# Kernel tuning notes

Hardware: AMD Instinct MI355X
Metric: run time of the kernel (lower is better)

Reference implementation:

```python
import jax, jax.numpy as jnp
import numpy as np

B, T, D, S = 32, 4096, 512, 256
SCALE = 0.1  # time_bias_scale


def setup_inputs() -> dict:
    key = jax.random.key(0)
    ks = jax.random.split(key, 9)
    return {
        "context": jax.random.normal(ks[0], (B, T, D), jnp.float32),
        "t_star": jax.random.uniform(ks[1], (B,), jnp.float32),
        "t_context": jax.random.uniform(ks[2], (B, T, 1), jnp.float32),
        "W1": jax.random.normal(ks[3], (1, D), jnp.float32) / np.sqrt(1.0),
        "b1": jax.random.normal(ks[4], (D,), jnp.float32) * 0.02,
        "W2": jax.random.normal(ks[5], (D, D), jnp.float32) / np.sqrt(D),
        "b2": jax.random.normal(ks[6], (D,), jnp.float32) * 0.02,
        "Wout": jax.random.normal(ks[7], (D, 2 * S), jnp.float32) / np.sqrt(D),
        "bout": jax.random.normal(ks[8], (2 * S,), jnp.float32) * 0.02,
    }


def reference(context, t_star, t_context, W1, b1, W2, b2, Wout, bout):
    # query embed: Linear(1,D) -> SiLU -> Linear(D,D)
    h = jax.nn.silu(t_star[:, None] @ W1 + b1)        # (B, D)
    q = h @ W2 + b2                                   # (B, D)
    # single-query attention scores with additive time bias
    scores = jnp.einsum('bd,btd->bt', q, context)     # (B, T)
    time_bias = -jnp.abs(t_star[:, None] - t_context[..., 0]) / SCALE  # (B, T)
    weights = jax.nn.softmax(scores + time_bias, axis=-1)
    pooled = jnp.einsum('bt,btd->bd', weights, context)  # (B, D)
    out = pooled @ Wout + bout                            # (B, 2S)
    mu, log_sigma = out[:, :S], out[:, S:]
    return (mu, log_sigma)
```

## Files before the change

### kernel.cpp

```cpp
#include <hip/hip_runtime.h>
#include <math.h>

#define BB 32
#define TT 4096
#define DD 512
#define SS 256
#define SEG 128
#define GRP 16
static constexpr float INV_SCALE = 10.0f;

__global__ __launch_bounds__(512) void k_q(
    const float* __restrict__ t_star, const float* __restrict__ W1,
    const float* __restrict__ b1, const float* __restrict__ W2,
    const float* __restrict__ b2, float* __restrict__ q) {
  const int b   = blockIdx.x >> 3;
  const int jg  = blockIdx.x & 7;
  const int tid = threadIdx.x;
  const int di  = tid & 63;
  const int kg  = tid >> 6;
  __shared__ float h[DD];
  __shared__ float red[8][64];
  {
    float x = t_star[b] * W1[tid] + b1[tid];
    h[tid] = x / (1.0f + __expf(-x));
  }
  __syncthreads();
  const float* w = W2 + jg * 64 + di;
  float acc = 0.0f;
#pragma unroll 8
  for (int kk = 0; kk < 64; ++kk) {
    const int k = kg * 64 + kk;
    acc += h[k] * w[(size_t)k * DD];
  }
  red[kg][di] = acc;
  __syncthreads();
  if (tid < 64) {
    float s = 0.0f;
#pragma unroll
    for (int g = 0; g < 8; ++g) s += red[g][tid];
    q[b * DD + jg * 64 + tid] = s + b2[jg * 64 + tid];
  }
}

#define GLDS(gp, lp)                                                        \
  __builtin_amdgcn_global_load_lds(                                         \
      (const __attribute__((address_space(1))) void*)(gp),                  \
      (__attribute__((address_space(3))) void*)(lp), 16, 0, 0)

__global__ __launch_bounds__(256) void k_fused(
    const float* __restrict__ ctx, const float* __restrict__ q,
    const float* __restrict__ t_star, const float* __restrict__ t_ctx,
    float* __restrict__ part_pool,
    float* __restrict__ part_ms) {
  __shared__ __align__(16) float lds[4][3][2 * DD];
  const int wid  = threadIdx.x >> 6;
  const int lane = threadIdx.x & 63;
  const int w    = blockIdx.x * 4 + wid;
  const int b    = w >> 7;
  const int s    = w & 127;

  const float4* qp = (const float4*)(q + b * DD);
  const float4 q0 = qp[lane];
  const float4 q1 = qp[64 + lane];
  const float ts = t_star[b];
  const float2 tc = *(const float2*)(t_ctx + b * TT + ((lane & 15) * 2 * SEG + 2 * s));
  const float tbx = -fabsf(ts - tc.x) * INV_SCALE;
  const float tby = -fabsf(ts - tc.y) * INV_SCALE;

  float m = -INFINITY, l = 0.0f;
  float4 p0 = {0, 0, 0, 0}, p1 = {0, 0, 0, 0};

  const float* cb = ctx + ((size_t)b * TT + 2 * s) * DD;

#pragma unroll
  for (int g = 0; g < 2; ++g) {
    const float* gb = cb + (size_t)g * 2 * SEG * DD;
    float* sb = &lds[wid][g][0];
#pragma unroll
    for (int piece = 0; piece < 4; ++piece)
      GLDS(gb + piece * 256 + lane * 4, sb + piece * 256);
  }

#pragma unroll
  for (int g = 0; g < GRP; ++g) {
    if (g + 2 < GRP) {
      const float* gb = cb + (size_t)(g + 2) * 2 * SEG * DD;
      float* sb = &lds[wid][(g + 2) % 3][0];
#pragma unroll
      for (int piece = 0; piece < 4; ++piece)
        GLDS(gb + piece * 256 + lane * 4, sb + piece * 256);
      asm volatile("s_waitcnt vmcnt(8)" ::: "memory");
    } else if (g + 1 < GRP) {
      asm volatile("s_waitcnt vmcnt(4)" ::: "memory");
    } else {
      asm volatile("s_waitcnt vmcnt(0)" ::: "memory");
    }

    const float4* sf = (const float4*)&lds[wid][g % 3][0];
    const float4 x0 = sf[lane];
    const float4 x1 = sf[64 + lane];
    const float4 y0 = sf[128 + lane];
    const float4 y1 = sf[192 + lane];

    float s0 = x0.x * q0.x + x0.y * q0.y + x0.z * q0.z + x0.w * q0.w +
               x1.x * q1.x + x1.y * q1.y + x1.z * q1.z + x1.w * q1.w;
    float s1 = y0.x * q0.x + y0.y * q0.y + y0.z * q0.z + y0.w * q0.w +
               y1.x * q1.x + y1.y * q1.y + y1.z * q1.z + y1.w * q1.w;
#pragma unroll
    for (int off = 32; off > 0; off >>= 1) {
      s0 += __shfl_xor(s0, off);
      s1 += __shfl_xor(s1, off);
    }
    s0 += __shfl(tbx, g);
    s1 += __shfl(tby, g);

    const float gm = fmaxf(s0, s1);
    const float nm = fmaxf(m, gm);
    const float sc = __expf(m - nm);
    m = nm;
    const float e0 = __expf(s0 - m);
    const float e1 = __expf(s1 - m);
    l = l * sc + e0 + e1;
    p0.x = p0.x * sc + e0 * x0.x + e1 * y0.x;
    p0.y = p0.y * sc + e0 * x0.y + e1 * y0.y;
    p0.z = p0.z * sc + e0 * x0.z + e1 * y0.z;
    p0.w = p0.w * sc + e0 * x0.w + e1 * y0.w;
    p1.x = p1.x * sc + e0 * x1.x + e1 * y1.x;
    p1.y = p1.y * sc + e0 * x1.y + e1 * y1.y;
    p1.z = p1.z * sc + e0 * x1.z + e1 * y1.z;
    p1.w = p1.w * sc + e0 * x1.w + e1 * y1.w;
  }

  float4* pp = (float4*)(part_pool + (size_t)w * DD);
  pp[lane] = p0;
  pp[64 + lane] = p1;
  if (lane == 0) {
    part_ms[w * 2 + 0] = m;
    part_ms[w * 2 + 1] = l;
  }
}

__global__ __launch_bounds__(512) void k_merge(
    const float* __restrict__ part_pool, const float* __restrict__ part_ms,
    float* __restrict__ pool) {
  const int b   = blockIdx.x >> 2;
  const int dg  = blockIdx.x & 3;
  const int tid = threadIdx.x;
  const int lane = tid & 63;
  const int base = b * SEG;
  __shared__ float scl[SEG];
  __shared__ float red[4][128];

  const float mA = part_ms[(base + lane) * 2 + 0];
  const float mB = part_ms[(base + 64 + lane) * 2 + 0];
  const float lA = part_ms[(base + lane) * 2 + 1];
  const float lB = part_ms[(base + 64 + lane) * 2 + 1];
  float M = fmaxf(mA, mB);
#pragma unroll
  for (int off = 32; off > 0; off >>= 1) M = fmaxf(M, __shfl_xor(M, off));
  float Z = __expf(mA - M) * lA + __expf(mB - M) * lB;
#pragma unroll
  for (int off = 32; off > 0; off >>= 1) Z += __shfl_xor(Z, off);
  const float invZ = 1.0f / Z;
  if (tid < SEG) scl[tid] = __expf(part_ms[(base + tid) * 2] - M);
  __syncthreads();

  const int dl = tid & 127;
  const int cg = tid >> 7;
  float acc = 0.0f;
#pragma unroll 8
  for (int i = 0; i < 32; ++i) {
    const int c = cg * 32 + i;
    acc += scl[c] * part_pool[((size_t)base + c) * DD + dg * 128 + dl];
  }
  red[cg][dl] = acc;
  __syncthreads();
  if (tid < 128)
    pool[b * DD + dg * 128 + tid] =
        (red[0][tid] + red[1][tid] + red[2][tid] + red[3][tid]) * invZ;
}

__global__ __launch_bounds__(256) void k_out(
    const float* __restrict__ pool, const float* __restrict__ Wout,
    const float* __restrict__ bout, float* __restrict__ out) {
  const int b   = blockIdx.x >> 3;
  const int jg  = blockIdx.x & 7;
  const int tid = threadIdx.x;
  const int kg  = tid >> 6;
  const int j   = tid & 63;
  const int jc  = jg * 64 + j;
  __shared__ float p[DD];
  __shared__ float red[4][64];

  p[tid] = pool[b * DD + tid];
  p[tid + 256] = pool[b * DD + 256 + tid];
  __syncthreads();

  float acc = 0.0f;
#pragma unroll 8
  for (int kk = 0; kk < 128; ++kk) {
    const int k = kg * 128 + kk;
    acc += p[k] * Wout[(size_t)k * DD + jc];
  }
  red[kg][j] = acc;
  __syncthreads();
  if (tid < 64) {
    const int jj = jg * 64 + tid;
    float o = red[0][tid] + red[1][tid] + red[2][tid] + red[3][tid] + bout[jj];
    if (jj < SS) out[b * SS + jj] = o;
    else         out[BB * SS + b * SS + (jj - SS)] = o;
  }
}

extern "C" void kernel_launch(void* const* d_in, const int* in_sizes, int n_in,
                              void* d_out, int out_size, void* d_ws, size_t ws_size,
                              hipStream_t stream) {
  const float* ctx    = (const float*)d_in[0];
  const float* t_star = (const float*)d_in[1];
  const float* t_ctx  = (const float*)d_in[2];
  const float* W1     = (const float*)d_in[3];
  const float* b1     = (const float*)d_in[4];
  const float* W2     = (const float*)d_in[5];
  const float* b2     = (const float*)d_in[6];
  const float* Wout   = (const float*)d_in[7];
  const float* bout   = (const float*)d_in[8];
  float* out = (float*)d_out;

  float* ws = (float*)d_ws;
  float* q         = ws;
  float* part_pool = q + (size_t)BB * DD;
  float* part_ms   = part_pool + (size_t)BB * SEG * DD;
  float* pool      = part_ms + (size_t)BB * SEG * 2;

  k_q<<<BB * 8, 512, 0, stream>>>(t_star, W1, b1, W2, b2, q);
  k_fused<<<BB * SEG / 4, 256, 0, stream>>>(ctx, q, t_star, t_ctx, part_pool, part_ms);
  k_merge<<<BB * 4, 512, 0, stream>>>(part_pool, part_ms, pool);
  k_out<<<BB * 8, 256, 0, stream>>>(pool, Wout, bout, out);
}
```

Baseline: 73.12 us.

## Process one context row per step with deeper 5-slot async prefetch pipeline

Each wave now handles one row per iteration instead of a pair, over 32 iterations, with a 5-slot LDS ring and 4 rows in flight instead of 3 slots holding pairs. Rows are strided by SEG instead of pairs strided by 2*SEG, and the time-bias lookup and vmcnt wait ladder change to match. The aim is smaller, more numerous in-flight loads and a simpler per-step softmax update. In exchange there are twice as many shuffle reductions and online-softmax rescales per row, and fewer bytes are in flight per wave.

Measured after the change: 76.51 us. 1.05x slower.

```diff
diff --git a/kernel.cpp b/kernel.cpp
--- a/kernel.cpp
+++ b/kernel.cpp
@@ -6,7 +6,7 @@
 #define DD 512
 #define SS 256
 #define SEG 128
-#define GRP 16
+#define GRP 32
 static constexpr float INV_SCALE = 10.0f;
 
 __global__ __launch_bounds__(512) void k_q(
@@ -52,7 +52,7 @@
     const float* __restrict__ t_star, const float* __restrict__ t_ctx,
     float* __restrict__ part_pool,
     float* __restrict__ part_ms) {
-  __shared__ __align__(16) float lds[4][3][2 * DD];
+  __shared__ __align__(16) float lds[4][5][DD];
   const int wid  = threadIdx.x >> 6;
   const int lane = threadIdx.x & 63;
   const int w    = blockIdx.x * 4 + wid;
@@ -63,72 +63,63 @@
   const float4 q0 = qp[lane];
   const float4 q1 = qp[64 + lane];
   const float ts = t_star[b];
-  const float2 tc = *(const float2*)(t_ctx + b * TT + ((lane & 15) * 2 * SEG + 2 * s));
-  const float tbx = -fabsf(ts - tc.x) * INV_SCALE;
-  const float tby = -fabsf(ts - tc.y) * INV_SCALE;
+  const float tcv = t_ctx[b * TT + (lane & 31) * SEG + s];
+  const float tb = -fabsf(ts - tcv) * INV_SCALE;
 
   float m = -INFINITY, l = 0.0f;
   float4 p0 = {0, 0, 0, 0}, p1 = {0, 0, 0, 0};
 
-  const float* cb = ctx + ((size_t)b * TT + 2 * s) * DD;
-
-#pragma unroll
-  for (int g = 0; g < 2; ++g) {
-    const float* gb = cb + (size_t)g * 2 * SEG * DD;
+  const float* cb = ctx + ((size_t)b * TT + s) * DD;
+
+#pragma unroll
+  for (int g = 0; g < 4; ++g) {
+    const float* gb = cb + (size_t)g * SEG * DD;
     float* sb = &lds[wid][g][0];
-#pragma unroll
-    for (int piece = 0; piece < 4; ++piece)
-      GLDS(gb + piece * 256 + lane * 4, sb + piece * 256);
+    GLDS(gb + lane * 4, sb);
+    GLDS(gb + 256 + lane * 4, sb + 256);
   }
 
 #pragma unroll
   for (int g = 0; g < GRP; ++g) {
-    if (g + 2 < GRP) {
-      const float* gb = cb + (size_t)(g + 2) * 2 * SEG * DD;
-      float* sb = &lds[wid][(g + 2) % 3][0];
-#pragma unroll
-      for (int piece = 0; piece < 4; ++piece)
-        GLDS(gb + piece * 256 + lane * 4, sb + piece * 256);
+    if (g + 4 < GRP) {
+      const float* gb = cb + (size_t)(g + 4) * SEG * DD;
+      float* sb = &lds[wid][(g + 4) % 5][0];
+      GLDS(gb + lane * 4, sb);
+      GLDS(gb + 256 + lane * 4, sb + 256);
       asm volatile("s_waitcnt vmcnt(8)" ::: "memory");
-    } else if (g + 1 < GRP) {
+    } else if (g + 4 == GRP) {
+      asm volatile("s_waitcnt vmcnt(6)" ::: "memory");
+    } else if (g + 4 == GRP + 1) {
       asm volatile("s_waitcnt vmcnt(4)" ::: "memory");
+    } else if (g + 4 == GRP + 2) {
+      asm volatile("s_waitcnt vmcnt(2)" ::: "memory");
     } else {
       asm volatile("s_waitcnt vmcnt(0)" ::: "memory");
     }
 
-    const float4* sf = (const float4*)&lds[wid][g % 3][0];
+    const float4* sf = (const float4*)&lds[wid][g % 5][0];
     const float4 x0 = sf[lane];
     const float4 x1 = sf[64 + lane];
-    const float4 y0 = sf[128 + lane];
-    const float4 y1 = sf[192 + lane];
-
-    float s0 = x0.x * q0.x + x0.y * q0.y + x0.z * q0.z + x0.w * q0.w +
-               x1.x * q1.x + x1.y * q1.y + x1.z * q1.z + x1.w * q1.w;
-    float s1 = y0.x * q0.x + y0.y * q0.y + y0.z * q0.z + y0.w * q0.w +
-               y1.x * q1.x + y1.y * q1.y + y1.z * q1.z + y1.w * q1.w;
-#pragma unroll
-    for (int off = 32; off > 0; off >>= 1) {
-      s0 += __shfl_xor(s0, off);
-      s1 += __shfl_xor(s1, off);
-    }
-    s0 += __shfl(tbx, g);
-    s1 += __shfl(tby, g);
-
-    const float gm = fmaxf(s0, s1);
-    const float nm = fmaxf(m, gm);
+
+    float a = x0.x * q0.x + x0.y * q0.y + x0.z * q0.z + x0.w * q0.w +
+              x1.x * q1.x + x1.y * q1.y + x1.z * q1.z + x1.w * q1.w;
+#pragma unroll
+    for (int off = 32; off > 0; off >>= 1) a += __shfl_xor(a, off);
+    a += __shfl(tb, g);
+
+    const float nm = fmaxf(m, a);
     const float sc = __expf(m - nm);
+    const float e  = __expf(a - nm);
     m = nm;
-    const float e0 = __expf(s0 - m);
-    const float e1 = __expf(s1 - m);
-    l = l * sc + e0 + e1;
-    p0.x = p0.x * sc + e0 * x0.x + e1 * y0.x;
-    p0.y = p0.y * sc + e0 * x0.y + e1 * y0.y;
-    p0.z = p0.z * sc + e0 * x0.z + e1 * y0.z;
-    p0.w = p0.w * sc + e0 * x0.w + e1 * y0.w;
-    p1.x = p1.x * sc + e0 * x1.x + e1 * y1.x;
-    p1.y = p1.y * sc + e0 * x1.y + e1 * y1.y;
-    p1.z = p1.z * sc + e0 * x1.z + e1 * y1.z;
-    p1.w = p1.w * sc + e0 * x1.w + e1 * y1.w;
+    l = l * sc + e;
+    p0.x = p0.x * sc + e * x0.x;
+    p0.y = p0.y * sc + e * x0.y;
+    p0.z = p0.z * sc + e * x0.z;
+    p0.w = p0.w * sc + e * x0.w;
+    p1.x = p1.x * sc + e * x1.x;
+    p1.y = p1.y * sc + e * x1.y;
+    p1.z = p1.z * sc + e * x1.z;
+    p1.w = p1.w * sc + e * x1.w;
   }
 
   float4* pp = (float4*)(part_pool + (size_t)w * DD);
```

## Split wave into half-waves per row with deferred softmax rescaling

Applied to the files above, without the earlier changes.

Each half-wave now processes one context row with 16 floats per lane, so the dot-product reduction needs 5 shuffle steps instead of 6 for two rows. Time biases are pre-broadcast into registers once, outside the loop. The online-softmax rescale is skipped unless the running max grows by more than a threshold, which removes most exp and multiply work per step. The two halves' accumulators are combined with a final cross-half shuffle. This costs more registers, adds a divergent branch, and risks overflow if scores grow by less than the threshold many times in a row.

Result: no change. 74.22 us (+1.5%).

```diff
diff --git a/kernel.cpp b/kernel.cpp
--- a/kernel.cpp
+++ b/kernel.cpp
@@ -8,6 +8,7 @@
 #define SEG 128
 #define GRP 16
 static constexpr float INV_SCALE = 10.0f;
+static constexpr float DEFER_THR = 28.0f;
 
 __global__ __launch_bounds__(512) void k_q(
     const float* __restrict__ t_star, const float* __restrict__ W1,
@@ -55,20 +56,28 @@
   __shared__ __align__(16) float lds[4][3][2 * DD];
   const int wid  = threadIdx.x >> 6;
   const int lane = threadIdx.x & 63;
+  const int li   = lane & 31;
+  const int half = lane >> 5;
   const int w    = blockIdx.x * 4 + wid;
   const int b    = w >> 7;
   const int s    = w & 127;
 
   const float4* qp = (const float4*)(q + b * DD);
-  const float4 q0 = qp[lane];
-  const float4 q1 = qp[64 + lane];
+  float4 qf[4];
+#pragma unroll
+  for (int k = 0; k < 4; ++k) qf[k] = qp[k * 32 + li];
+
   const float ts = t_star[b];
-  const float2 tc = *(const float2*)(t_ctx + b * TT + ((lane & 15) * 2 * SEG + 2 * s));
-  const float tbx = -fabsf(ts - tc.x) * INV_SCALE;
-  const float tby = -fabsf(ts - tc.y) * INV_SCALE;
+  const float tcv = t_ctx[b * TT + 2 * (li * SEG + s) + half];
+  const float tb = -fabsf(ts - tcv) * INV_SCALE;
+  float myb[GRP];
+#pragma unroll
+  for (int g = 0; g < GRP; ++g) myb[g] = __shfl(tb, (lane & 32) + g);
 
   float m = -INFINITY, l = 0.0f;
-  float4 p0 = {0, 0, 0, 0}, p1 = {0, 0, 0, 0};
+  float4 p[4];
+#pragma unroll
+  for (int k = 0; k < 4; ++k) p[k] = {0, 0, 0, 0};
 
   const float* cb = ctx + ((size_t)b * TT + 2 * s) * DD;
 
@@ -90,50 +99,58 @@
       for (int piece = 0; piece < 4; ++piece)
         GLDS(gb + piece * 256 + lane * 4, sb + piece * 256);
       asm volatile("s_waitcnt vmcnt(8)" ::: "memory");
-    } else if (g + 1 < GRP) {
+    } else if (g + 2 == GRP) {
       asm volatile("s_waitcnt vmcnt(4)" ::: "memory");
     } else {
       asm volatile("s_waitcnt vmcnt(0)" ::: "memory");
     }
 
-    const float4* sf = (const float4*)&lds[wid][g % 3][0];
-    const float4 x0 = sf[lane];
-    const float4 x1 = sf[64 + lane];
-    const float4 y0 = sf[128 + lane];
-    const float4 y1 = sf[192 + lane];
-
-    float s0 = x0.x * q0.x + x0.y * q0.y + x0.z * q0.z + x0.w * q0.w +
-               x1.x * q1.x + x1.y * q1.y + x1.z * q1.z + x1.w * q1.w;
-    float s1 = y0.x * q0.x + y0.y * q0.y + y0.z * q0.z + y0.w * q0.w +
-               y1.x * q1.x + y1.y * q1.y + y1.z * q1.z + y1.w * q1.w;
-#pragma unroll
-    for (int off = 32; off > 0; off >>= 1) {
-      s0 += __shfl_xor(s0, off);
-      s1 += __shfl_xor(s1, off);
+    const float4* sf = (const float4*)(&lds[wid][g % 3][0] + half * DD);
+    float4 x[4];
+#pragma unroll
+    for (int k = 0; k < 4; ++k) x[k] = sf[k * 32 + li];
+
+    float a = x[0].x * qf[0].x + x[0].y * qf[0].y + x[0].z * qf[0].z + x[0].w * qf[0].w;
+#pragma unroll
+    for (int k = 1; k < 4; ++k)
+      a += x[k].x * qf[k].x + x[k].y * qf[k].y + x[k].z * qf[k].z + x[k].w * qf[k].w;
+#pragma unroll
+    for (int off = 16; off > 0; off >>= 1) a += __shfl_xor(a, off);
+    a += myb[g];
+
+    const float pm = fmaxf(a, __shfl_xor(a, 32));
+    if (pm > m + DEFER_THR) {
+      const float sc = __expf(m - pm);
+      m = pm;
+      l *= sc;
+#pragma unroll
+      for (int k = 0; k < 4; ++k) {
+        p[k].x *= sc; p[k].y *= sc; p[k].z *= sc; p[k].w *= sc;
+      }
     }
-    s0 += __shfl(tbx, g);
-    s1 += __shfl(tby, g);
-
-    const float gm = fmaxf(s0, s1);
-    const float nm = fmaxf(m, gm);
-    const float sc = __expf(m - nm);
-    m = nm;
-    const float e0 = __expf(s0 - m);
-    const float e1 = __expf(s1 - m);
-    l = l * sc + e0 + e1;
-    p0.x = p0.x * sc + e0 * x0.x + e1 * y0.x;
-    p0.y = p0.y * sc + e0 * x0.y + e1 * y0.y;
-    p0.z = p0.z * sc + e0 * x0.z + e1 * y0.z;
-    p0.w = p0.w * sc + e0 * x0.w + e1 * y0.w;
-    p1.x = p1.x * sc + e0 * x1.x + e1 * y1.x;
-    p1.y = p1.y * sc + e0 * x1.y + e1 * y1.y;
-    p1.z = p1.z * sc + e0 * x1.z + e1 * y1.z;
-    p1.w = p1.w * sc + e0 * x1.w + e1 * y1.w;
-  }
-
-  float4* pp = (float4*)(part_pool + (size_t)w * DD);
-  pp[lane] = p0;
-  pp[64 + lane] = p1;
+    const float e = __expf(a - m);
+    l += e;
+#pragma unroll
+    for (int k = 0; k < 4; ++k) {
+      p[k].x += e * x[k].x; p[k].y += e * x[k].y;
+      p[k].z += e * x[k].z; p[k].w += e * x[k].w;
+    }
+  }
+
+  l += __shfl_xor(l, 32);
+#pragma unroll
+  for (int k = 0; k < 4; ++k) {
+    p[k].x += __shfl_xor(p[k].x, 32);
+    p[k].y += __shfl_xor(p[k].y, 32);
+    p[k].z += __shfl_xor(p[k].z, 32);
+    p[k].w += __shfl_xor(p[k].w, 32);
+  }
+
+  if (lane < 32) {
+    float4* pp = (float4*)(part_pool + (size_t)w * DD);
+#pragma unroll
+    for (int k = 0; k < 4; ++k) pp[k * 32 + li] = p[k];
+  }
   if (lane == 0) {
     part_ms[w * 2 + 0] = m;
     part_ms[w * 2 + 1] = l;
```
